# Kernel optimization log

Hardware: AMD Instinct MI355X
Metric: run time of the kernel (lower is better)

Reference implementation:

```python
import jax, jax.numpy as jnp
import numpy as np

N_NODES = 50000
N_EDGES = 1600000
HEADS = 4
EMB = 16          # per-head output features
HIDDEN = 256
BATCH = 1024
IN_FEAT = 4       # num_node_features (hard-coded in source)
NEG_SLOPE = 0.2   # PyG GATConv default leaky_relu slope


def setup_inputs() -> dict:
    key = jax.random.key(0)
    ks = jax.random.split(key, 8)
    out_dim = HEADS * EMB
    return {
        "message": jax.random.normal(ks[0], (BATCH, HIDDEN), dtype=jnp.float32),
        "x": jax.random.normal(ks[1], (N_NODES, IN_FEAT), dtype=jnp.float32),
        "edge_index": jax.random.randint(ks[2], (2, N_EDGES), 0, N_NODES, dtype=jnp.int64)
                      if jax.config.read("jax_enable_x64") else
                      jax.random.randint(ks[2], (2, N_EDGES), 0, N_NODES, dtype=jnp.int32),
        "gat_w": jax.random.normal(ks[3], (IN_FEAT, out_dim), dtype=jnp.float32) * 0.5,
        "att_src": jax.random.normal(ks[4], (HEADS, EMB), dtype=jnp.float32) * 0.25,
        "att_dst": jax.random.normal(ks[5], (HEADS, EMB), dtype=jnp.float32) * 0.25,
        "gat_b": jnp.zeros((out_dim,), dtype=jnp.float32),
        "fc_w": jax.random.normal(ks[6], (HIDDEN, out_dim), dtype=jnp.float32) * (1.0 / np.sqrt(HIDDEN)),
        "fc_b": jnp.zeros((out_dim,), dtype=jnp.float32),
    }


def reference(message, x, edge_index, gat_w, att_src, att_dst, gat_b, fc_w, fc_b):
    N = x.shape[0]
    H, F = att_src.shape
    src, dst = edge_index[0], edge_index[1]

    # --- GATConv (single layer, concat heads) ---
    h = (x @ gat_w).reshape(N, H, F)                       # [N,H,F]
    a_s = jnp.einsum('nhf,hf->nh', h, att_src)             # per-node src score
    a_d = jnp.einsum('nhf,hf->nh', h, att_dst)             # per-node dst score
    e = jax.nn.leaky_relu(a_s[src] + a_d[dst], NEG_SLOPE)  # [E,H]

    # stable softmax over edges grouped by destination node
    m = jax.ops.segment_max(e, dst, num_segments=N)        # [N,H]
    ex = jnp.exp(e - m[dst])                               # [E,H]
    denom = jax.ops.segment_sum(ex, dst, num_segments=N)   # [N,H]
    alpha = ex / (denom[dst] + 1e-16)                      # [E,H]

    # weighted aggregation of source features into destinations
    agg = jax.ops.segment_sum(alpha[:, :, None] * h[src], dst, num_segments=N)  # [N,H,F]
    h_out = agg.reshape(N, H * F) + gat_b                  # [N, H*F]

    # --- fc + matmul + log_softmax ---
    msg_emb = message @ fc_w + fc_b                        # [B, H*F]
    logits = (h_out @ msg_emb.T).T                         # [B, N]
    return jax.nn.log_softmax(logits, axis=1)
```

## Files before the change

### kernel.cpp

```cpp
#include <hip/hip_runtime.h>
#include <math.h>

#define N_NODES 50000
#define N_EDGES 1600000
#define HEADS 4
#define EMB 16
#define HOUT 64
#define HIDDEN 256
#define BATCH 1024
#define NEG_SLOPE 0.2f
#define ATS 50176
#define CHK 512
#define NCH 98
#define SCAN_NB 196
#define NXCD 8
#define DRANGE 6250

__device__ __forceinline__ float lrelu(float x) { return x > 0.f ? x : NEG_SLOPE * x; }

__global__ void k_msgemb(const float* __restrict__ msg, const float* __restrict__ fcw,
                         const float* __restrict__ fcb, const float* __restrict__ gatb,
                         float* __restrict__ msg_emb, float* __restrict__ msgT,
                         float* __restrict__ cvec) {
    __shared__ float mrow[HIDDEN];
    int b = blockIdx.x;
    int j = threadIdx.x;
    for (int k = j; k < HIDDEN; k += 64) mrow[k] = msg[b * HIDDEN + k];
    __syncthreads();
    float acc = fcb[j];
    #pragma unroll 8
    for (int k = 0; k < HIDDEN; k++) acc += mrow[k] * fcw[k * HOUT + j];
    msg_emb[b * HOUT + j] = acc;
    msgT[j * BATCH + b] = acc;
    float cv = gatb[j] * acc;
    for (int o = 32; o > 0; o >>= 1) cv += __shfl_down(cv, o);
    if (j == 0) cvec[b] = cv;
}

__global__ void k_node(const float* __restrict__ x, const float* __restrict__ gatw,
                       const float* __restrict__ atts, const float* __restrict__ attd,
                       float* __restrict__ h, float* __restrict__ a_s, float* __restrict__ a_d) {
    int tid = blockIdx.x * blockDim.x + threadIdx.x;
    int n = tid >> 6;
    int j = tid & 63;
    if (n >= N_NODES) return;
    float4 xv = ((const float4*)x)[n];
    float hv = xv.x * gatw[j] + xv.y * gatw[64 + j] + xv.z * gatw[128 + j] + xv.w * gatw[192 + j];
    h[n * 64 + j] = hv;
    float s = hv * atts[j];
    float d = hv * attd[j];
    for (int o = 8; o > 0; o >>= 1) {
        s += __shfl_down(s, o, 16);
        d += __shfl_down(d, o, 16);
    }
    if ((j & 15) == 0) {
        int head = j >> 4;
        a_s[n * 4 + head] = s;
        a_d[n * 4 + head] = d;
    }
}

__global__ void k_count(const int* __restrict__ ei, int* __restrict__ cnt) {
    int p = blockIdx.x & 7;
    int tile = blockIdx.x >> 3;
    int e = tile * 256 + threadIdx.x;
    if (e < N_EDGES) {
        int d = ei[N_EDGES + e];
        if ((unsigned)(d - p * DRANGE) < (unsigned)DRANGE)
            atomicAdd(&cnt[d], 1);
    }
}

__global__ void k_scan1(const int* __restrict__ cnt, int* __restrict__ localx,
                        int* __restrict__ partial) {
    int b = blockIdx.x, t = threadIdx.x;
    int i = b * 256 + t;
    int v = (i < N_NODES) ? cnt[i] : 0;
    int lane = t & 63, w = t >> 6;
    int sv = v;
    #pragma unroll
    for (int o = 1; o < 64; o <<= 1) {
        int u = __shfl_up(sv, o);
        if (lane >= o) sv += u;
    }
    __shared__ int wsums[4];
    if (lane == 63) wsums[w] = sv;
    __syncthreads();
    int woff = 0;
    #pragma unroll
    for (int k = 0; k < 4; k++) woff += (k < w) ? wsums[k] : 0;
    if (i < N_NODES) localx[i] = woff + sv - v;
    if (t == 0) partial[b] = wsums[0] + wsums[1] + wsums[2] + wsums[3];
}

__global__ void k_scan2(const int* __restrict__ partial, int* __restrict__ blockoff,
                        int* __restrict__ rowptr_last) {
    int t = threadIdx.x;
    int v = (t < SCAN_NB) ? partial[t] : 0;
    int lane = t & 63, w = t >> 6;
    int sv = v;
    #pragma unroll
    for (int o = 1; o < 64; o <<= 1) {
        int u = __shfl_up(sv, o);
        if (lane >= o) sv += u;
    }
    __shared__ int wsums[4];
    if (lane == 63) wsums[w] = sv;
    __syncthreads();
    int woff = 0;
    #pragma unroll
    for (int k = 0; k < 4; k++) woff += (k < w) ? wsums[k] : 0;
    int excl = woff + sv - v;
    if (t < SCAN_NB) blockoff[t] = excl;
    if (t == 255) rowptr_last[0] = excl + v;
}

__global__ void k_scan3(const int* __restrict__ localx, const int* __restrict__ blockoff,
                        int* __restrict__ rowptr, int* __restrict__ cursor) {
    int i = blockIdx.x * 256 + threadIdx.x;
    if (i < N_NODES) {
        int r = localx[i] + blockoff[blockIdx.x];
        rowptr[i] = r;
        cursor[i] = r;
    }
}

__global__ void k_scatter(const int* __restrict__ ei, int* __restrict__ cursor, int* __restrict__ csr) {
    int p = blockIdx.x & 7;
    int tile = blockIdx.x >> 3;
    int e = tile * 256 + threadIdx.x;
    if (e < N_EDGES) {
        int d = ei[N_EDGES + e];
        if ((unsigned)(d - p * DRANGE) < (unsigned)DRANGE) {
            int pos = atomicAdd(&cursor[d], 1);
            csr[pos] = ei[e];
        }
    }
}

__global__ __launch_bounds__(256, 8) void k_agg(const int* __restrict__ rowptr,
                      const int* __restrict__ csr,
                      const float* __restrict__ a_s, const float* __restrict__ a_d,
                      const float* __restrict__ h, float* __restrict__ agg) {
    __shared__ float salpha[4][64];
    int wid = threadIdx.x >> 6;
    int lane = threadIdx.x & 63;
    int n = blockIdx.x * 4 + wid;
    if (n >= N_NODES) return;
    int beg = rowptr[n], end = rowptr[n + 1];
    int head = lane & 3, eoff = lane >> 2;
    float adh = a_d[n * 4 + head];

    float s = 0.f;
    for (int i = beg + eoff; i < end; i += 16) {
        int src = csr[i];
        s += __expf(lrelu(a_s[src * 4 + head] + adh));
    }
    #pragma unroll
    for (int o = 4; o < 64; o <<= 1) s += __shfl_xor(s, o);
    float inv = 1.f / (s + 1e-16f);

    float acc = 0.f;
    const float* ap = &salpha[wid][(lane >> 4) * 16];
    for (int base = beg; base < end; base += 16) {
        int e = base + eoff;
        int ec = (e < end) ? e : (end - 1);
        int src = csr[ec];
        float ev = lrelu(a_s[src * 4 + head] + adh);
        float alpha = (e < end) ? __expf(ev) * inv : 0.f;
        salpha[wid][head * 16 + eoff] = alpha;
        __builtin_amdgcn_wave_barrier();
        #pragma unroll
        for (int c = 0; c < 4; c++) {
            float4 av = *(const float4*)(ap + c * 4);
            int s0 = __builtin_amdgcn_readlane(src, c * 16 + 0);
            int s1 = __builtin_amdgcn_readlane(src, c * 16 + 4);
            int s2 = __builtin_amdgcn_readlane(src, c * 16 + 8);
            int s3 = __builtin_amdgcn_readlane(src, c * 16 + 12);
            acc = fmaf(av.x, h[(size_t)s0 * 64 + lane], acc);
            acc = fmaf(av.y, h[(size_t)s1 * 64 + lane], acc);
            acc = fmaf(av.z, h[(size_t)s2 * 64 + lane], acc);
            acc = fmaf(av.w, h[(size_t)s3 * 64 + lane], acc);
        }
        __builtin_amdgcn_wave_barrier();
    }
    agg[(size_t)n * 64 + lane] = acc;
}

__global__ void k_transpose(const float* __restrict__ agg, float* __restrict__ aggT) {
    __shared__ float tile[64][65];
    int t = threadIdx.x;
    int n0 = blockIdx.x * 64;
    #pragma unroll
    for (int i = 0; i < 16; i++) {
        int idx = i * 256 + t;
        int nl = idx >> 6, f = idx & 63;
        int n = n0 + nl;
        tile[nl][f] = (n < N_NODES) ? agg[(size_t)n * 64 + f] : 0.f;
    }
    __syncthreads();
    int c = n0 >> 9;
    int nb = n0 & 511;
    #pragma unroll
    for (int i = 0; i < 16; i++) {
        int idx = i * 256 + t;
        int f = idx >> 6, nl = idx & 63;
        aggT[(size_t)c * (64 * CHK) + f * CHK + nb + nl] = tile[nl][f];
    }
}

__global__ __launch_bounds__(256, 6) void k_logsum(const float* __restrict__ aggT,
    const float* __restrict__ msgT, const float* __restrict__ cvec,
    float* __restrict__ ps) {
    __shared__ float red_s[16][4];
    int t = threadIdx.x;
    int bg = blockIdx.x;
    int chunk = blockIdx.y;
    const float* ap = aggT + (size_t)chunk * (64 * CHK) + 2 * t;
    const float* mp = msgT + bg * 16;

    float acc0[16], acc1[16];
    #pragma unroll
    for (int b = 0; b < 16; b++) { acc0[b] = 0.f; acc1[b] = 0.f; }

    #pragma unroll 4
    for (int k = 0; k < 64; k++) {
        float2 av = *(const float2*)(ap + (size_t)k * CHK);
        const float* mrow = mp + k * BATCH;
        #pragma unroll
        for (int b = 0; b < 16; b++) {
            float m = mrow[b];
            acc0[b] = fmaf(av.x, m, acc0[b]);
            acc1[b] = fmaf(av.y, m, acc1[b]);
        }
    }

    int n = chunk * CHK + 2 * t;
    bool valid = (n < N_NODES);
    int lane = t & 63, w = t >> 6;
    #pragma unroll
    for (int b = 0; b < 16; b++) {
        int bglob = bg * 16 + b;
        float sc = cvec[bglob];
        float ls = 0.f;
        if (valid) ls = __expf(acc0[b] + sc) + __expf(acc1[b] + sc);
        #pragma unroll
        for (int o = 1; o < 64; o <<= 1) ls += __shfl_xor(ls, o);
        if (lane == 0) red_s[b][w] = ls;
    }
    __syncthreads();
    if (t < 16) {
        float S = red_s[t][0] + red_s[t][1] + red_s[t][2] + red_s[t][3];
        ps[(bg * 16 + t) * NCH + chunk] = S;
    }
}

__global__ void k_rowstats(const float* __restrict__ ps, float* __restrict__ rowls) {
    int b = blockIdx.x * blockDim.x + threadIdx.x;
    if (b >= BATCH) return;
    float S = 0.f;
    for (int i = 0; i < NCH; i++) S += ps[b * NCH + i];
    rowls[b] = logf(S);
}

__global__ __launch_bounds__(256, 6) void k_logits_w(const float* __restrict__ aggT,
    const float* __restrict__ msgT, const float* __restrict__ cvec,
    const float* __restrict__ rowls, float* __restrict__ out) {
    int t = threadIdx.x;
    int bg = blockIdx.x;
    int chunk = blockIdx.y;
    const float* ap = aggT + (size_t)chunk * (64 * CHK) + 2 * t;
    const float* mp = msgT + bg * 16;

    float acc0[16], acc1[16];
    #pragma unroll
    for (int b = 0; b < 16; b++) { acc0[b] = 0.f; acc1[b] = 0.f; }

    #pragma unroll 4
    for (int k = 0; k < 64; k++) {
        float2 av = *(const float2*)(ap + (size_t)k * CHK);
        const float* mrow = mp + k * BATCH;
        #pragma unroll
        for (int b = 0; b < 16; b++) {
            float m = mrow[b];
            acc0[b] = fmaf(av.x, m, acc0[b]);
            acc1[b] = fmaf(av.y, m, acc1[b]);
        }
    }

    int n = chunk * CHK + 2 * t;
    if (n >= N_NODES) return;
    #pragma unroll
    for (int b = 0; b < 16; b++) {
        int bglob = bg * 16 + b;
        float sub = cvec[bglob] - rowls[bglob];
        *(float2*)(out + (size_t)bglob * N_NODES + n) =
            make_float2(acc0[b] + sub, acc1[b] + sub);
    }
}

extern "C" void kernel_launch(void* const* d_in, const int* in_sizes, int n_in,
                              void* d_out, int out_size, void* d_ws, size_t ws_size,
                              hipStream_t stream) {
    const float* message = (const float*)d_in[0];
    const float* x       = (const float*)d_in[1];
    const int*   ei      = (const int*)d_in[2];
    const float* gat_w   = (const float*)d_in[3];
    const float* att_src = (const float*)d_in[4];
    const float* att_dst = (const float*)d_in[5];
    const float* gat_b   = (const float*)d_in[6];
    const float* fc_w    = (const float*)d_in[7];
    const float* fc_b    = (const float*)d_in[8];
    float* out = (float*)d_out;

    float* ws      = (float*)d_ws;
    float* msg_emb = ws;
    float* msgT    = msg_emb + BATCH * HOUT;
    float* cvec    = msgT + HOUT * BATCH;
    float* a_s     = cvec + BATCH;
    float* a_d     = a_s + (size_t)N_NODES * HEADS;
    float* agg     = a_d + (size_t)N_NODES * HEADS;
    float* hbuf    = agg + (size_t)N_NODES * HOUT;
    float* aggT    = hbuf;
    float* ps      = hbuf + (size_t)HOUT * ATS;
    float* rowls   = ps + BATCH * NCH;
    int*   cnt     = (int*)(rowls + BATCH);
    int*   rowptr  = cnt + N_NODES;
    int*   cursor  = rowptr + N_NODES + 1;
    int*   csr     = cursor + N_NODES;
    int*   localx  = csr + N_EDGES;
    int*   partial = localx + N_NODES;
    int*   blockoff= partial + SCAN_NB;

    hipMemsetAsync(cnt, 0, N_NODES * sizeof(int), stream);
    k_msgemb<<<BATCH, 64, 0, stream>>>(message, fc_w, fc_b, gat_b, msg_emb, msgT, cvec);
    k_node<<<(N_NODES * 64 + 255) / 256, 256, 0, stream>>>(x, gat_w, att_src, att_dst, hbuf, a_s, a_d);
    k_count<<<NXCD * (N_EDGES / 256), 256, 0, stream>>>(ei, cnt);
    k_scan1<<<SCAN_NB, 256, 0, stream>>>(cnt, localx, partial);
    k_scan2<<<1, 256, 0, stream>>>(partial, blockoff, rowptr + N_NODES);
    k_scan3<<<SCAN_NB, 256, 0, stream>>>(localx, blockoff, rowptr, cursor);
    k_scatter<<<NXCD * (N_EDGES / 256), 256, 0, stream>>>(ei, cursor, csr);
    k_agg<<<(N_NODES + 3) / 4, 256, 0, stream>>>(rowptr, csr, a_s, a_d, hbuf, agg);
    k_transpose<<<ATS / 64, 256, 0, stream>>>(agg, aggT);
    dim3 g4(64, NCH);
    k_logsum<<<g4, 256, 0, stream>>>(aggT, msgT, cvec, ps);
    k_rowstats<<<4, 256, 0, stream>>>(ps, rowls);
    k_logits_w<<<g4, 256, 0, stream>>>(aggT, msgT, cvec, rowls, out);
}
```

Baseline: 602.5 us.

## Use split-bf16 MFMA for logits GEMMs and drop transpose and bias term

Both logit GEMM passes now run on bf16 32x32x16 MFMA instructions instead of scalar FP32 FMAs. Near-fp32 accuracy is kept by splitting each operand into hi and lo bf16 parts and issuing three MFMAs per k-step. k_agg writes the hi/lo halves row-major directly, so the transpose kernel and its extra buffer pass go away. The per-batch gat_b·msg constant is dropped because it cancels in log_softmax. The risks are reduced precision from the split-bf16 scheme and strided output stores from the MFMA result layout.

```diff
diff --git a/kernel.cpp b/kernel.cpp
--- a/kernel.cpp
+++ b/kernel.cpp
@@ -10,18 +10,26 @@
 #define BATCH 1024
 #define NEG_SLOPE 0.2f
 #define ATS 50176
-#define CHK 512
-#define NCH 98
 #define SCAN_NB 196
 #define NXCD 8
 #define DRANGE 6250
+#define NSTRIP 196
+#define NT32 1563
+
+typedef __attribute__((ext_vector_type(8))) short bf16x8;
+typedef __attribute__((ext_vector_type(16))) float f32x16;
 
 __device__ __forceinline__ float lrelu(float x) { return x > 0.f ? x : NEG_SLOPE * x; }
 
+__device__ __forceinline__ ushort f2bf(float f) {
+    unsigned u = __float_as_uint(f);
+    return (ushort)((u + 0x7fffu + ((u >> 16) & 1u)) >> 16);
+}
+__device__ __forceinline__ float bf2f(ushort h) { return __uint_as_float(((unsigned)h) << 16); }
+
 __global__ void k_msgemb(const float* __restrict__ msg, const float* __restrict__ fcw,
-                         const float* __restrict__ fcb, const float* __restrict__ gatb,
-                         float* __restrict__ msg_emb, float* __restrict__ msgT,
-                         float* __restrict__ cvec) {
+                         const float* __restrict__ fcb,
+                         ushort* __restrict__ msg_hi, ushort* __restrict__ msg_lo) {
     __shared__ float mrow[HIDDEN];
     int b = blockIdx.x;
     int j = threadIdx.x;
@@ -30,11 +38,9 @@
     float acc = fcb[j];
     #pragma unroll 8
     for (int k = 0; k < HIDDEN; k++) acc += mrow[k] * fcw[k * HOUT + j];
-    msg_emb[b * HOUT + j] = acc;
-    msgT[j * BATCH + b] = acc;
-    float cv = gatb[j] * acc;
-    for (int o = 32; o > 0; o >>= 1) cv += __shfl_down(cv, o);
-    if (j == 0) cvec[b] = cv;
+    ushort hi = f2bf(acc);
+    msg_hi[b * HOUT + j] = hi;
+    msg_lo[b * HOUT + j] = f2bf(acc - bf2f(hi));
 }
 
 __global__ void k_node(const float* __restrict__ x, const float* __restrict__ gatw,
@@ -141,7 +147,8 @@
 __global__ __launch_bounds__(256, 8) void k_agg(const int* __restrict__ rowptr,
                       const int* __restrict__ csr,
                       const float* __restrict__ a_s, const float* __restrict__ a_d,
-                      const float* __restrict__ h, float* __restrict__ agg) {
+                      const float* __restrict__ h,
+                      ushort* __restrict__ agg_hi, ushort* __restrict__ agg_lo) {
     __shared__ float salpha[4][64];
     int wid = threadIdx.x >> 6;
     int lane = threadIdx.x & 63;
@@ -184,74 +191,68 @@
         }
         __builtin_amdgcn_wave_barrier();
     }
-    agg[(size_t)n * 64 + lane] = acc;
-}
-
-__global__ void k_transpose(const float* __restrict__ agg, float* __restrict__ aggT) {
-    __shared__ float tile[64][65];
+    ushort hi = f2bf(acc);
+    agg_hi[(size_t)n * 64 + lane] = hi;
+    agg_lo[(size_t)n * 64 + lane] = f2bf(acc - bf2f(hi));
+}
+
+
+__global__ __launch_bounds__(256, 4) void k_logsum(const ushort* __restrict__ agg_hi,
+    const ushort* __restrict__ agg_lo, const ushort* __restrict__ msg_hi,
+    const ushort* __restrict__ msg_lo, float* __restrict__ ps) {
     int t = threadIdx.x;
-    int n0 = blockIdx.x * 64;
-    #pragma unroll
-    for (int i = 0; i < 16; i++) {
-        int idx = i * 256 + t;
-        int nl = idx >> 6, f = idx & 63;
-        int n = n0 + nl;
-        tile[nl][f] = (n < N_NODES) ? agg[(size_t)n * 64 + f] : 0.f;
-    }
-    __syncthreads();
-    int c = n0 >> 9;
-    int nb = n0 & 511;
-    #pragma unroll
-    for (int i = 0; i < 16; i++) {
-        int idx = i * 256 + t;
-        int f = idx >> 6, nl = idx & 63;
-        aggT[(size_t)c * (64 * CHK) + f * CHK + nb + nl] = tile[nl][f];
-    }
-}
-
-__global__ __launch_bounds__(256, 6) void k_logsum(const float* __restrict__ aggT,
-    const float* __restrict__ msgT, const float* __restrict__ cvec,
-    float* __restrict__ ps) {
-    __shared__ float red_s[16][4];
-    int t = threadIdx.x;
-    int bg = blockIdx.x;
-    int chunk = blockIdx.y;
-    const float* ap = aggT + (size_t)chunk * (64 * CHK) + 2 * t;
-    const float* mp = msgT + bg * 16;
-
-    float acc0[16], acc1[16];
-    #pragma unroll
-    for (int b = 0; b < 16; b++) { acc0[b] = 0.f; acc1[b] = 0.f; }
-
-    #pragma unroll 4
-    for (int k = 0; k < 64; k++) {
-        float2 av = *(const float2*)(ap + (size_t)k * CHK);
-        const float* mrow = mp + k * BATCH;
-        #pragma unroll
-        for (int b = 0; b < 16; b++) {
-            float m = mrow[b];
-            acc0[b] = fmaf(av.x, m, acc0[b]);
-            acc1[b] = fmaf(av.y, m, acc1[b]);
-        }
-    }
-
-    int n = chunk * CHK + 2 * t;
-    bool valid = (n < N_NODES);
-    int lane = t & 63, w = t >> 6;
-    #pragma unroll
-    for (int b = 0; b < 16; b++) {
-        int bglob = bg * 16 + b;
-        float sc = cvec[bglob];
-        float ls = 0.f;
-        if (valid) ls = __expf(acc0[b] + sc) + __expf(acc1[b] + sc);
-        #pragma unroll
-        for (int o = 1; o < 64; o <<= 1) ls += __shfl_xor(ls, o);
-        if (lane == 0) red_s[b][w] = ls;
-    }
-    __syncthreads();
-    if (t < 16) {
-        float S = red_s[t][0] + red_s[t][1] + red_s[t][2] + red_s[t][3];
-        ps[(bg * 16 + t) * NCH + chunk] = S;
+    int lane = t & 63, wid = t >> 6;
+    int l31 = lane & 31, half = lane >> 5;
+    int b0 = blockIdx.y * 32;
+    int gw = blockIdx.x * 4 + wid;
+
+    const ushort* mh = msg_hi + (size_t)(b0 + l31) * HOUT + half * 8;
+    const ushort* ml = msg_lo + (size_t)(b0 + l31) * HOUT + half * 8;
+    bf16x8 mH[4], mL[4];
+    #pragma unroll
+    for (int ks = 0; ks < 4; ks++) {
+        mH[ks] = *(const bf16x8*)(mh + ks * 16);
+        mL[ks] = *(const bf16x8*)(ml + ks * 16);
+    }
+
+    float sacc[16];
+    #pragma unroll
+    for (int r = 0; r < 16; r++) sacc[r] = 0.f;
+
+    for (int i = 0; i < 8; i++) {
+        int tile = gw * 8 + i;
+        int n0 = tile * 32;
+        if (n0 >= N_NODES) break;
+        const ushort* ah = agg_hi + (size_t)(n0 + l31) * HOUT + half * 8;
+        const ushort* al = agg_lo + (size_t)(n0 + l31) * HOUT + half * 8;
+        f32x16 acc;
+        #pragma unroll
+        for (int r = 0; r < 16; r++) acc[r] = 0.f;
+        #pragma unroll
+        for (int ks = 0; ks < 4; ks++) {
+            bf16x8 aH = *(const bf16x8*)(ah + ks * 16);
+            bf16x8 aL = *(const bf16x8*)(al + ks * 16);
+            acc = __builtin_amdgcn_mfma_f32_32x32x16_bf16(mH[ks], aH, acc, 0, 0, 0);
+            acc = __builtin_amdgcn_mfma_f32_32x32x16_bf16(mH[ks], aL, acc, 0, 0, 0);
+            acc = __builtin_amdgcn_mfma_f32_32x32x16_bf16(mL[ks], aH, acc, 0, 0, 0);
+        }
+        bool valid = (n0 + l31) < N_NODES;
+        #pragma unroll
+        for (int r = 0; r < 16; r++) sacc[r] += valid ? __expf(acc[r]) : 0.f;
+    }
+    #pragma unroll
+    for (int r = 0; r < 16; r++) {
+        float s = sacc[r];
+        #pragma unroll
+        for (int o = 1; o < 32; o <<= 1) s += __shfl_xor(s, o);
+        sacc[r] = s;
+    }
+    if (l31 == 0) {
+        #pragma unroll
+        for (int r = 0; r < 16; r++) {
+            int b = b0 + (r & 3) + 8 * (r >> 2) + 4 * half;
+            ps[(size_t)b * NSTRIP + gw] = sacc[r];
+        }
     }
 }
 
@@ -259,43 +260,59 @@
     int b = blockIdx.x * blockDim.x + threadIdx.x;
     if (b >= BATCH) return;
     float S = 0.f;
-    for (int i = 0; i < NCH; i++) S += ps[b * NCH + i];
+    for (int i = 0; i < NSTRIP; i++) S += ps[b * NSTRIP + i];
     rowls[b] = logf(S);
 }
 
-__global__ __launch_bounds__(256, 6) void k_logits_w(const float* __restrict__ aggT,
-    const float* __restrict__ msgT, const float* __restrict__ cvec,
-    const float* __restrict__ rowls, float* __restrict__ out) {
+__global__ __launch_bounds__(256, 4) void k_logits_w(const ushort* __restrict__ agg_hi,
+    const ushort* __restrict__ agg_lo, const ushort* __restrict__ msg_hi,
+    const ushort* __restrict__ msg_lo, const float* __restrict__ rowls,
+    float* __restrict__ out) {
     int t = threadIdx.x;
-    int bg = blockIdx.x;
-    int chunk = blockIdx.y;
-    const float* ap = aggT + (size_t)chunk * (64 * CHK) + 2 * t;
-    const float* mp = msgT + bg * 16;
-
-    float acc0[16], acc1[16];
-    #pragma unroll
-    for (int b = 0; b < 16; b++) { acc0[b] = 0.f; acc1[b] = 0.f; }
-
-    #pragma unroll 4
-    for (int k = 0; k < 64; k++) {
-        float2 av = *(const float2*)(ap + (size_t)k * CHK);
-        const float* mrow = mp + k * BATCH;
-        #pragma unroll
-        for (int b = 0; b < 16; b++) {
-            float m = mrow[b];
-            acc0[b] = fmaf(av.x, m, acc0[b]);
-            acc1[b] = fmaf(av.y, m, acc1[b]);
-        }
-    }
-
-    int n = chunk * CHK + 2 * t;
-    if (n >= N_NODES) return;
-    #pragma unroll
-    for (int b = 0; b < 16; b++) {
-        int bglob = bg * 16 + b;
-        float sub = cvec[bglob] - rowls[bglob];
-        *(float2*)(out + (size_t)bglob * N_NODES + n) =
-            make_float2(acc0[b] + sub, acc1[b] + sub);
+    int lane = t & 63, wid = t >> 6;
+    int l31 = lane & 31, half = lane >> 5;
+    int b0 = blockIdx.y * 32;
+    int gw = blockIdx.x * 4 + wid;
+
+    const ushort* mh = msg_hi + (size_t)(b0 + l31) * HOUT + half * 8;
+    const ushort* ml = msg_lo + (size_t)(b0 + l31) * HOUT + half * 8;
+    bf16x8 mH[4], mL[4];
+    #pragma unroll
+    for (int ks = 0; ks < 4; ks++) {
+        mH[ks] = *(const bf16x8*)(mh + ks * 16);
+        mL[ks] = *(const bf16x8*)(ml + ks * 16);
+    }
+    float sub[16];
+    int brow[16];
+    #pragma unroll
+    for (int r = 0; r < 16; r++) {
+        brow[r] = b0 + (r & 3) + 8 * (r >> 2) + 4 * half;
+        sub[r] = rowls[brow[r]];
+    }
+
+    for (int i = 0; i < 8; i++) {
+        int tile = gw * 8 + i;
+        int n0 = tile * 32;
+        if (n0 >= N_NODES) break;
+        const ushort* ah = agg_hi + (size_t)(n0 + l31) * HOUT + half * 8;
+        const ushort* al = agg_lo + (size_t)(n0 + l31) * HOUT + half * 8;
+        f32x16 acc;
+        #pragma unroll
+        for (int r = 0; r < 16; r++) acc[r] = 0.f;
+        #pragma unroll
+        for (int ks = 0; ks < 4; ks++) {
+            bf16x8 aH = *(const bf16x8*)(ah + ks * 16);
+            bf16x8 aL = *(const bf16x8*)(al + ks * 16);
+            acc = __builtin_amdgcn_mfma_f32_32x32x16_bf16(mH[ks], aH, acc, 0, 0, 0);
+            acc = __builtin_amdgcn_mfma_f32_32x32x16_bf16(mH[ks], aL, acc, 0, 0, 0);
+            acc = __builtin_amdgcn_mfma_f32_32x32x16_bf16(mL[ks], aH, acc, 0, 0, 0);
+        }
+        int n = n0 + l31;
+        if (n < N_NODES) {
+            #pragma unroll
+            for (int r = 0; r < 16; r++)
+                out[(size_t)brow[r] * N_NODES + n] = acc[r] - sub[r];
+        }
     }
 }
 
@@ -308,23 +325,21 @@
     const float* gat_w   = (const float*)d_in[3];
     const float* att_src = (const float*)d_in[4];
     const float* att_dst = (const float*)d_in[5];
-    const float* gat_b   = (const float*)d_in[6];
     const float* fc_w    = (const float*)d_in[7];
     const float* fc_b    = (const float*)d_in[8];
     float* out = (float*)d_out;
 
     float* ws      = (float*)d_ws;
-    float* msg_emb = ws;
-    float* msgT    = msg_emb + BATCH * HOUT;
-    float* cvec    = msgT + HOUT * BATCH;
-    float* a_s     = cvec + BATCH;
+    float* a_s     = ws;
     float* a_d     = a_s + (size_t)N_NODES * HEADS;
-    float* agg     = a_d + (size_t)N_NODES * HEADS;
-    float* hbuf    = agg + (size_t)N_NODES * HOUT;
-    float* aggT    = hbuf;
-    float* ps      = hbuf + (size_t)HOUT * ATS;
-    float* rowls   = ps + BATCH * NCH;
-    int*   cnt     = (int*)(rowls + BATCH);
+    float* hbuf    = a_d + (size_t)N_NODES * HEADS;
+    float* ps      = hbuf + (size_t)N_NODES * HOUT;
+    float* rowls   = ps + (size_t)BATCH * NSTRIP;
+    ushort* msg_hi = (ushort*)(rowls + BATCH);
+    ushort* msg_lo = msg_hi + (size_t)BATCH * HOUT;
+    ushort* agg_hi = msg_lo + (size_t)BATCH * HOUT;
+    ushort* agg_lo = agg_hi + (size_t)ATS * HOUT;
+    int*   cnt     = (int*)(agg_lo + (size_t)ATS * HOUT);
     int*   rowptr  = cnt + N_NODES;
     int*   cursor  = rowptr + N_NODES + 1;
     int*   csr     = cursor + N_NODES;
@@ -333,17 +348,16 @@
     int*   blockoff= partial + SCAN_NB;
 
     hipMemsetAsync(cnt, 0, N_NODES * sizeof(int), stream);
-    k_msgemb<<<BATCH, 64, 0, stream>>>(message, fc_w, fc_b, gat_b, msg_emb, msgT, cvec);
+    k_msgemb<<<BATCH, 64, 0, stream>>>(message, fc_w, fc_b, msg_hi, msg_lo);
     k_node<<<(N_NODES * 64 + 255) / 256, 256, 0, stream>>>(x, gat_w, att_src, att_dst, hbuf, a_s, a_d);
     k_count<<<NXCD * (N_EDGES / 256), 256, 0, stream>>>(ei, cnt);
     k_scan1<<<SCAN_NB, 256, 0, stream>>>(cnt, localx, partial);
     k_scan2<<<1, 256, 0, stream>>>(partial, blockoff, rowptr + N_NODES);
     k_scan3<<<SCAN_NB, 256, 0, stream>>>(localx, blockoff, rowptr, cursor);
     k_scatter<<<NXCD * (N_EDGES / 256), 256, 0, stream>>>(ei, cursor, csr);
-    k_agg<<<(N_NODES + 3) / 4, 256, 0, stream>>>(rowptr, csr, a_s, a_d, hbuf, agg);
-    k_transpose<<<ATS / 64, 256, 0, stream>>>(agg, aggT);
-    dim3 g4(64, NCH);
-    k_logsum<<<g4, 256, 0, stream>>>(aggT, msgT, cvec, ps);
+    k_agg<<<(N_NODES + 3) / 4, 256, 0, stream>>>(rowptr, csr, a_s, a_d, hbuf, agg_hi, agg_lo);
+    dim3 g4(49, 32);
+    k_logsum<<<g4, 256, 0, stream>>>(agg_hi, agg_lo, msg_hi, msg_lo, ps);
     k_rowstats<<<4, 256, 0, stream>>>(ps, rowls);
-    k_logits_w<<<g4, 256, 0, stream>>>(aggT, msgT, cvec, rowls, out);
-}
+    k_logits_w<<<g4, 256, 0, stream>>>(agg_hi, agg_lo, msg_hi, msg_lo, rowls, out);
+}
```

New measurement: 608.6 us. No clear change (+1.0%).
